# Kernel optimization log

Measured on AMD Instinct MI355X. Metric: run time of the kernel, lower is better.

## Reference

```python
import jax, jax.numpy as jnp
import numpy as np

B, P, E, S = 4, 2048, 4096, 16


def setup_inputs() -> dict:
    key = jax.random.key(0)
    ks = jax.random.split(key, 6)
    return {
        "x": jax.random.normal(ks[0], (B, P, E), dtype=jnp.float32),
        "product": jax.random.normal(ks[1], (P, S), dtype=jnp.float32) * 0.1,
        "person": jax.random.normal(ks[2], (E, S), dtype=jnp.float32) * 0.1,
        "W1": jax.random.normal(ks[3], (2 * S, S), dtype=jnp.float32) * (1.0 / np.sqrt(2 * S)),
        "W2": jax.random.normal(ks[4], (S, S), dtype=jnp.float32) * (1.0 / np.sqrt(S)),
        "W3": jax.random.normal(ks[5], (S, 1), dtype=jnp.float32) * (1.0 / np.sqrt(S)),
    }


def reference(x, product, person, W1, W2, W3):
    # cartesian product concat([pr, pe]) @ W1 == pr @ W1[:S] + pe @ W1[S:]
    # (no bias), so we avoid materializing the (P*E, 2S) concat tensor.
    Wa, Wb = W1[:S], W1[S:]           # each (S, S)
    h1 = jnp.tanh(
        (product @ Wa)[:, None, :] +  # (P, 1, S)
        (person @ Wb)[None, :, :]     # (1, E, S)
    )                                  # (P, E, S)
    h2 = jnp.tanh(h1 @ W2)            # (P, E, S)
    z = (h2 @ W3)[..., 0]             # (P, E)
    score = jnp.where(z >= 0, z, 0.1 * z)  # leaky relu, alpha=0.1
    return score[None, :, :] * x      # (B, P, E)
```

## Files before the change

kernel.cpp:

```cpp
#include <hip/hip_runtime.h>

#define BB 4
#define PP 2048
#define EE 4096
#define SS 16
#define TP 16
#define EBLK 256

typedef __fp16 v2h __attribute__((ext_vector_type(2)));
typedef __fp16 v4h __attribute__((ext_vector_type(4)));
typedef float  v4f __attribute__((ext_vector_type(4)));

static __device__ __forceinline__ float tanh_poly(float x) {
    float t = x * x;
    float u = fmaf(0.010163f, t, -0.046163f);
    u = fmaf(u, t, 0.130718f);
    u = fmaf(u, t, -0.332932f);
    u = fmaf(u, t, 0.999980f);
    return x * u;
}

__global__ __launch_bounds__(256) void precompute_ab(
    const float* __restrict__ product, const float* __restrict__ person,
    const float* __restrict__ W1, float* __restrict__ a, float* __restrict__ b)
{
    int row = blockIdx.x * blockDim.x + threadIdx.x;
    if (row >= PP + EE) return;
    const bool  is_p  = row < PP;
    const float* in   = is_p ? (product + (size_t)row * SS)
                             : (person  + (size_t)(row - PP) * SS);
    const float* W    = is_p ? W1 : (W1 + SS * SS);
    float*       orow = is_p ? (a + (size_t)row * SS)
                             : (b + (size_t)(row - PP) * SS);
    float v[SS];
#pragma unroll
    for (int k = 0; k < SS; ++k) v[k] = in[k];
#pragma unroll
    for (int j = 0; j < SS; ++j) {
        float acc = 0.0f;
#pragma unroll
        for (int k = 0; k < SS; ++k) acc = fmaf(v[k], W[k * SS + j], acc);
        orow[j] = acc;
    }
}

__global__ __launch_bounds__(256) void score_mul(
    const float* __restrict__ x, const float* __restrict__ a,
    const float* __restrict__ b, const float* __restrict__ W2,
    const float* __restrict__ W3, float* __restrict__ out)
{
    const int tid  = threadIdx.x;
    const int lane = tid & 63;
    const int n    = lane & 15;
    const int q    = lane >> 4;
    const int q0   = q & 1;
    const int q1   = q >> 1;

    const int eown  = blockIdx.x * EBLK + tid;
    const int ebase = blockIdx.x * EBLK + (tid & ~63);
    const int p0 = blockIdx.y * TP;

    const size_t PLANE = (size_t)PP * EE;

    float4 brg[4];
#pragma unroll
    for (int g = 0; g < 4; ++g)
        brg[g] = *(const float4*)(b + (size_t)(ebase + g*16 + n) * SS + q*4);

    v4h w2a;
    {
        v2h lo = __builtin_amdgcn_cvt_pkrtz(W2[(q*4+0)*SS + n], W2[(q*4+1)*SS + n]);
        v2h hi = __builtin_amdgcn_cvt_pkrtz(W2[(q*4+2)*SS + n], W2[(q*4+3)*SS + n]);
        w2a[0]=lo[0]; w2a[1]=lo[1]; w2a[2]=hi[0]; w2a[3]=hi[1];
    }

    float4 w3v = ((const float4*)W3)[q];
    const float w3r[4] = {w3v.x, w3v.y, w3v.z, w3v.w};

    size_t base0 = (size_t)p0 * EE + (size_t)eown;
    const float* __restrict__ xp0 = x   + base0;
    float*       __restrict__ op0 = out + base0;

    const v4f z4 = {0.f, 0.f, 0.f, 0.f};

    float xv[BB];
#pragma unroll
    for (int bb2 = 0; bb2 < BB; ++bb2)
        xv[bb2] = xp0[(size_t)bb2 * PLANE];
    float4 av = *(const float4*)(a + (size_t)p0 * SS + q*4);

    for (int ip = 0; ip < TP; ++ip) {
        const size_t off = (size_t)ip * EE;

        float  xn[BB];
        float4 an;
        if (ip + 1 < TP) {
            const size_t offn = off + EE;
#pragma unroll
            for (int bb2 = 0; bb2 < BB; ++bb2)
                xn[bb2] = xp0[(size_t)bb2 * PLANE + offn];
            an = *(const float4*)(a + (size_t)(p0 + ip + 1) * SS + q*4);
        } else {
            an = av;
#pragma unroll
            for (int bb2 = 0; bb2 < BB; ++bb2) xn[bb2] = xv[bb2];
        }

        v4h bfrag[4];
#pragma unroll
        for (int g = 0; g < 4; ++g) {
            float t0 = tanh_poly(av.x + brg[g].x);
            float t1 = tanh_poly(av.y + brg[g].y);
            float t2 = tanh_poly(av.z + brg[g].z);
            float t3 = tanh_poly(av.w + brg[g].w);
            v2h lo = __builtin_amdgcn_cvt_pkrtz(t0, t1);
            v2h hi = __builtin_amdgcn_cvt_pkrtz(t2, t3);
            bfrag[g][0]=lo[0]; bfrag[g][1]=lo[1]; bfrag[g][2]=hi[0]; bfrag[g][3]=hi[1];
        }

        float P[4];
#pragma unroll
        for (int g = 0; g < 4; ++g) {
            v4f acc = __builtin_amdgcn_mfma_f32_16x16x16f16(w2a, bfrag[g], z4, 0, 0, 0);
            float s = 0.f;
#pragma unroll
            for (int r = 0; r < 4; ++r)
                s = fmaf(tanh_poly(acc[r]), w3r[r], s);
            P[g] = s;
        }

        float S1[2];
#pragma unroll
        for (int g1 = 0; g1 < 2; ++g1) {
            float send = q0 ? P[2*g1 + 0] : P[2*g1 + 1];
            float keep = q0 ? P[2*g1 + 1] : P[2*g1 + 0];
            S1[g1] = keep + __shfl_xor(send, 16);
        }
        {
            float send = q1 ? S1[0] : S1[1];
            float keep = q1 ? S1[1] : S1[0];
            float z = keep + __shfl_xor(send, 32);

            float sc = fmaxf(z, 0.f) + 0.1f * fminf(z, 0.f);

#pragma unroll
            for (int bb2 = 0; bb2 < BB; ++bb2)
                __builtin_nontemporal_store(sc * xv[bb2],
                                            op0 + (size_t)bb2 * PLANE + off);
        }

        av = an;
#pragma unroll
        for (int bb2 = 0; bb2 < BB; ++bb2) xv[bb2] = xn[bb2];
    }
}

extern "C" void kernel_launch(void* const* d_in, const int* in_sizes, int n_in,
                              void* d_out, int out_size, void* d_ws, size_t ws_size,
                              hipStream_t stream)
{
    const float* x       = (const float*)d_in[0];
    const float* product = (const float*)d_in[1];
    const float* person  = (const float*)d_in[2];
    const float* W1      = (const float*)d_in[3];
    const float* W2      = (const float*)d_in[4];
    const float* W3      = (const float*)d_in[5];
    float* out = (float*)d_out;

    float* a = (float*)d_ws;
    float* b = a + (size_t)PP * SS;

    dim3 g1((PP + EE + 255) / 256);
    precompute_ab<<<g1, 256, 0, stream>>>(product, person, W1, a, b);

    dim3 g2(EE / EBLK, PP / TP);
    score_mul<<<g2, 256, 0, stream>>>(x, a, b, W2, W3, out);
}
```

Baseline: 270.1 us.

## Process two product rows per iteration, drop software prefetch and nontemporal stores

The main loop now handles two p rows per iteration, loading both rows' x values up front and interleaving the tanh, MFMA and shuffle chains for the two rows to expose more independent work. The explicit one-ahead register prefetch of x and a is removed, and output writes change from nontemporal stores to ordinary stores. This trades the explicit pipelining for more instruction-level parallelism within each iteration, at the cost of higher register pressure. The ordinary stores may also pollute the cache on a streaming output.

```diff
diff --git a/kernel.cpp b/kernel.cpp
--- a/kernel.cpp
+++ b/kernel.cpp
@@ -71,7 +71,7 @@
     {
         v2h lo = __builtin_amdgcn_cvt_pkrtz(W2[(q*4+0)*SS + n], W2[(q*4+1)*SS + n]);
         v2h hi = __builtin_amdgcn_cvt_pkrtz(W2[(q*4+2)*SS + n], W2[(q*4+3)*SS + n]);
-        w2a[0]=lo[0]; w2a[1]=lo[1]; w2a[2]=hi[0]; w2a[3]=hi[1];
+        w2a = __builtin_shufflevector(lo, hi, 0, 1, 2, 3);
     }
 
     float4 w3v = ((const float4*)W3)[q];
@@ -83,75 +83,80 @@
 
     const v4f z4 = {0.f, 0.f, 0.f, 0.f};
 
-    float xv[BB];
+    for (int ip = 0; ip < TP; ip += 2) {
+        const size_t offA = (size_t)ip * EE;
+        const size_t offB = offA + EE;
+
+        float xA[BB], xB[BB];
 #pragma unroll
-    for (int bb2 = 0; bb2 < BB; ++bb2)
-        xv[bb2] = xp0[(size_t)bb2 * PLANE];
-    float4 av = *(const float4*)(a + (size_t)p0 * SS + q*4);
-
-    for (int ip = 0; ip < TP; ++ip) {
-        const size_t off = (size_t)ip * EE;
-
-        float  xn[BB];
-        float4 an;
-        if (ip + 1 < TP) {
-            const size_t offn = off + EE;
-#pragma unroll
-            for (int bb2 = 0; bb2 < BB; ++bb2)
-                xn[bb2] = xp0[(size_t)bb2 * PLANE + offn];
-            an = *(const float4*)(a + (size_t)(p0 + ip + 1) * SS + q*4);
-        } else {
-            an = av;
-#pragma unroll
-            for (int bb2 = 0; bb2 < BB; ++bb2) xn[bb2] = xv[bb2];
+        for (int bb2 = 0; bb2 < BB; ++bb2) {
+            xA[bb2] = xp0[(size_t)bb2 * PLANE + offA];
+            xB[bb2] = xp0[(size_t)bb2 * PLANE + offB];
         }
 
-        v4h bfrag[4];
+        float4 avA = *(const float4*)(a + (size_t)(p0 + ip)     * SS + q*4);
+        float4 avB = *(const float4*)(a + (size_t)(p0 + ip + 1) * SS + q*4);
+
+        v4h bfA[4], bfB[4];
 #pragma unroll
         for (int g = 0; g < 4; ++g) {
-            float t0 = tanh_poly(av.x + brg[g].x);
-            float t1 = tanh_poly(av.y + brg[g].y);
-            float t2 = tanh_poly(av.z + brg[g].z);
-            float t3 = tanh_poly(av.w + brg[g].w);
-            v2h lo = __builtin_amdgcn_cvt_pkrtz(t0, t1);
-            v2h hi = __builtin_amdgcn_cvt_pkrtz(t2, t3);
-            bfrag[g][0]=lo[0]; bfrag[g][1]=lo[1]; bfrag[g][2]=hi[0]; bfrag[g][3]=hi[1];
+            float a0 = tanh_poly(avA.x + brg[g].x);
+            float a1 = tanh_poly(avA.y + brg[g].y);
+            float a2 = tanh_poly(avA.z + brg[g].z);
+            float a3 = tanh_poly(avA.w + brg[g].w);
+            v2h alo = __builtin_amdgcn_cvt_pkrtz(a0, a1);
+            v2h ahi = __builtin_amdgcn_cvt_pkrtz(a2, a3);
+            bfA[g] = __builtin_shufflevector(alo, ahi, 0, 1, 2, 3);
+
+            float b0 = tanh_poly(avB.x + brg[g].x);
+            float b1 = tanh_poly(avB.y + brg[g].y);
+            float b2 = tanh_poly(avB.z + brg[g].z);
+            float b3 = tanh_poly(avB.w + brg[g].w);
+            v2h blo = __builtin_amdgcn_cvt_pkrtz(b0, b1);
+            v2h bhi = __builtin_amdgcn_cvt_pkrtz(b2, b3);
+            bfB[g] = __builtin_shufflevector(blo, bhi, 0, 1, 2, 3);
         }
 
-        float P[4];
+        float PA[4], PB[4];
 #pragma unroll
         for (int g = 0; g < 4; ++g) {
-            v4f acc = __builtin_amdgcn_mfma_f32_16x16x16f16(w2a, bfrag[g], z4, 0, 0, 0);
-            float s = 0.f;
+            v4f accA = __builtin_amdgcn_mfma_f32_16x16x16f16(w2a, bfA[g], z4, 0, 0, 0);
+            v4f accB = __builtin_amdgcn_mfma_f32_16x16x16f16(w2a, bfB[g], z4, 0, 0, 0);
+            float sA = 0.f, sB = 0.f;
 #pragma unroll
-            for (int r = 0; r < 4; ++r)
-                s = fmaf(tanh_poly(acc[r]), w3r[r], s);
-            P[g] = s;
+            for (int r = 0; r < 4; ++r) {
+                sA = fmaf(tanh_poly(accA[r]), w3r[r], sA);
+                sB = fmaf(tanh_poly(accB[r]), w3r[r], sB);
+            }
+            PA[g] = sA;
+            PB[g] = sB;
         }
 
-        float S1[2];
+        float S1A[2], S1B[2];
 #pragma unroll
         for (int g1 = 0; g1 < 2; ++g1) {
-            float send = q0 ? P[2*g1 + 0] : P[2*g1 + 1];
-            float keep = q0 ? P[2*g1 + 1] : P[2*g1 + 0];
-            S1[g1] = keep + __shfl_xor(send, 16);
+            float sendA = q0 ? PA[2*g1 + 0] : PA[2*g1 + 1];
+            float keepA = q0 ? PA[2*g1 + 1] : PA[2*g1 + 0];
+            S1A[g1] = keepA + __shfl_xor(sendA, 16);
+            float sendB = q0 ? PB[2*g1 + 0] : PB[2*g1 + 1];
+            float keepB = q0 ? PB[2*g1 + 1] : PB[2*g1 + 0];
+            S1B[g1] = keepB + __shfl_xor(sendB, 16);
         }
-        {
-            float send = q1 ? S1[0] : S1[1];
-            float keep = q1 ? S1[1] : S1[0];
-            float z = keep + __shfl_xor(send, 32);
+        float sendA = q1 ? S1A[0] : S1A[1];
+        float keepA = q1 ? S1A[1] : S1A[0];
+        float zA    = keepA + __shfl_xor(sendA, 32);
+        float sendB = q1 ? S1B[0] : S1B[1];
+        float keepB = q1 ? S1B[1] : S1B[0];
+        float zB    = keepB + __shfl_xor(sendB, 32);
 
-            float sc = fmaxf(z, 0.f) + 0.1f * fminf(z, 0.f);
+        float scA = fmaxf(zA, 0.f) + 0.1f * fminf(zA, 0.f);
+        float scB = fmaxf(zB, 0.f) + 0.1f * fminf(zB, 0.f);
 
 #pragma unroll
-            for (int bb2 = 0; bb2 < BB; ++bb2)
-                __builtin_nontemporal_store(sc * xv[bb2],
-                                            op0 + (size_t)bb2 * PLANE + off);
+        for (int bb2 = 0; bb2 < BB; ++bb2) {
+            op0[(size_t)bb2 * PLANE + offA] = scA * xA[bb2];
+            op0[(size_t)bb2 * PLANE + offB] = scB * xB[bb2];
         }
-
-        av = an;
-#pragma unroll
-        for (int bb2 = 0; bb2 < BB; ++bb2) xv[bb2] = xn[bb2];
     }
 }
 
```

Result: faster. 262.0 us (-3.0%).

## Widen per-thread work to four elements with float4 loads and stores

Applied to the files above, without the earlier changes.

Each wave now covers 256 E columns (16 MFMA groups) instead of 64, and each thread handles 4 consecutive E elements. x loads and out stores become float4 vectorized, with a lane-shuffle redistribution of scores. The b fragments are stored as fp16 to save registers, TP drops to 8, and an occupancy hint is added. The software prefetch of x is removed and nontemporal stores are replaced by plain stores. The change trades more shuffles and lower b precision for wider memory transactions.

```diff
diff --git a/kernel.cpp b/kernel.cpp
--- a/kernel.cpp
+++ b/kernel.cpp
@@ -4,8 +4,8 @@
 #define PP 2048
 #define EE 4096
 #define SS 16
-#define TP 16
-#define EBLK 256
+#define TP 8
+#define EPB 1024
 
 typedef __fp16 v2h __attribute__((ext_vector_type(2)));
 typedef __fp16 v4h __attribute__((ext_vector_type(4)));
@@ -44,114 +44,115 @@
     }
 }
 
-__global__ __launch_bounds__(256) void score_mul(
+__global__ __launch_bounds__(256, 4) void score_mul(
     const float* __restrict__ x, const float* __restrict__ a,
     const float* __restrict__ b, const float* __restrict__ W2,
     const float* __restrict__ W3, float* __restrict__ out)
 {
     const int tid  = threadIdx.x;
     const int lane = tid & 63;
+    const int wid  = tid >> 6;
     const int n    = lane & 15;
     const int q    = lane >> 4;
     const int q0   = q & 1;
     const int q1   = q >> 1;
 
-    const int eown  = blockIdx.x * EBLK + tid;
-    const int ebase = blockIdx.x * EBLK + (tid & ~63);
-    const int p0 = blockIdx.y * TP;
-
+    const int ebase = blockIdx.x * EPB + wid * 256;
+    const int e0    = ebase + lane * 4;
+    const int p0    = blockIdx.y * TP;
     const size_t PLANE = (size_t)PP * EE;
 
-    float4 brg[4];
+    v4h brg[16];
 #pragma unroll
-    for (int g = 0; g < 4; ++g)
-        brg[g] = *(const float4*)(b + (size_t)(ebase + g*16 + n) * SS + q*4);
+    for (int g = 0; g < 16; ++g) {
+        float4 bv = *(const float4*)(b + (size_t)(ebase + g*16 + n) * SS + q*4);
+        v2h lo = __builtin_amdgcn_cvt_pkrtz(bv.x, bv.y);
+        v2h hi = __builtin_amdgcn_cvt_pkrtz(bv.z, bv.w);
+        brg[g] = __builtin_shufflevector(lo, hi, 0, 1, 2, 3);
+    }
 
     v4h w2a;
     {
         v2h lo = __builtin_amdgcn_cvt_pkrtz(W2[(q*4+0)*SS + n], W2[(q*4+1)*SS + n]);
         v2h hi = __builtin_amdgcn_cvt_pkrtz(W2[(q*4+2)*SS + n], W2[(q*4+3)*SS + n]);
-        w2a[0]=lo[0]; w2a[1]=lo[1]; w2a[2]=hi[0]; w2a[3]=hi[1];
+        w2a = __builtin_shufflevector(lo, hi, 0, 1, 2, 3);
     }
 
-    float4 w3v = ((const float4*)W3)[q];
-    const float w3r[4] = {w3v.x, w3v.y, w3v.z, w3v.w};
+    const float4 w3v = ((const float4*)W3)[q];
 
-    size_t base0 = (size_t)p0 * EE + (size_t)eown;
-    const float* __restrict__ xp0 = x   + base0;
-    float*       __restrict__ op0 = out + base0;
+    const float* __restrict__ xp0 = x   + (size_t)p0 * EE + e0;
+    float*       __restrict__ op0 = out + (size_t)p0 * EE + e0;
 
-    const v4f z4 = {0.f, 0.f, 0.f, 0.f};
-
-    float xv[BB];
-#pragma unroll
-    for (int bb2 = 0; bb2 < BB; ++bb2)
-        xv[bb2] = xp0[(size_t)bb2 * PLANE];
-    float4 av = *(const float4*)(a + (size_t)p0 * SS + q*4);
+    const v4f zero4 = {0.f, 0.f, 0.f, 0.f};
+    const int srcb = ((lane >> 2) & 3) * 16 + (lane & 3) * 4;
 
     for (int ip = 0; ip < TP; ++ip) {
         const size_t off = (size_t)ip * EE;
 
-        float  xn[BB];
-        float4 an;
-        if (ip + 1 < TP) {
-            const size_t offn = off + EE;
+        float4 av = *(const float4*)(a + (size_t)(p0 + ip) * SS + q*4);
+
+        float4 xv[BB];
 #pragma unroll
-            for (int bb2 = 0; bb2 < BB; ++bb2)
-                xn[bb2] = xp0[(size_t)bb2 * PLANE + offn];
-            an = *(const float4*)(a + (size_t)(p0 + ip + 1) * SS + q*4);
-        } else {
-            an = av;
+        for (int bb2 = 0; bb2 < BB; ++bb2)
+            xv[bb2] = *(const float4*)(xp0 + (size_t)bb2 * PLANE + off);
+
+        float P[16];
 #pragma unroll
-            for (int bb2 = 0; bb2 < BB; ++bb2) xn[bb2] = xv[bb2];
-        }
-
-        v4h bfrag[4];
-#pragma unroll
-        for (int g = 0; g < 4; ++g) {
-            float t0 = tanh_poly(av.x + brg[g].x);
-            float t1 = tanh_poly(av.y + brg[g].y);
-            float t2 = tanh_poly(av.z + brg[g].z);
-            float t3 = tanh_poly(av.w + brg[g].w);
+        for (int g = 0; g < 16; ++g) {
+            float t0 = tanh_poly(av.x + (float)brg[g][0]);
+            float t1 = tanh_poly(av.y + (float)brg[g][1]);
+            float t2 = tanh_poly(av.z + (float)brg[g][2]);
+            float t3 = tanh_poly(av.w + (float)brg[g][3]);
             v2h lo = __builtin_amdgcn_cvt_pkrtz(t0, t1);
             v2h hi = __builtin_amdgcn_cvt_pkrtz(t2, t3);
-            bfrag[g][0]=lo[0]; bfrag[g][1]=lo[1]; bfrag[g][2]=hi[0]; bfrag[g][3]=hi[1];
-        }
-
-        float P[4];
-#pragma unroll
-        for (int g = 0; g < 4; ++g) {
-            v4f acc = __builtin_amdgcn_mfma_f32_16x16x16f16(w2a, bfrag[g], z4, 0, 0, 0);
+            v4h bf = __builtin_shufflevector(lo, hi, 0, 1, 2, 3);
+            v4f acc = __builtin_amdgcn_mfma_f32_16x16x16f16(w2a, bf, zero4, 0, 0, 0);
             float s = 0.f;
-#pragma unroll
-            for (int r = 0; r < 4; ++r)
-                s = fmaf(tanh_poly(acc[r]), w3r[r], s);
+            s = fmaf(tanh_poly(acc[0]), w3v.x, s);
+            s = fmaf(tanh_poly(acc[1]), w3v.y, s);
+            s = fmaf(tanh_poly(acc[2]), w3v.z, s);
+            s = fmaf(tanh_poly(acc[3]), w3v.w, s);
             P[g] = s;
         }
 
-        float S1[2];
+        float S1[8];
 #pragma unroll
-        for (int g1 = 0; g1 < 2; ++g1) {
-            float send = q0 ? P[2*g1 + 0] : P[2*g1 + 1];
-            float keep = q0 ? P[2*g1 + 1] : P[2*g1 + 0];
-            S1[g1] = keep + __shfl_xor(send, 16);
+        for (int m = 0; m < 8; ++m) {
+            float send = q0 ? P[2*m]   : P[2*m+1];
+            float keep = q0 ? P[2*m+1] : P[2*m];
+            S1[m] = keep + __shfl_xor(send, 16);
         }
-        {
-            float send = q1 ? S1[0] : S1[1];
-            float keep = q1 ? S1[1] : S1[0];
-            float z = keep + __shfl_xor(send, 32);
+        float F[4];
+#pragma unroll
+        for (int c = 0; c < 4; ++c) {
+            float send = q1 ? S1[2*c]   : S1[2*c+1];
+            float keep = q1 ? S1[2*c+1] : S1[2*c];
+            F[c] = keep + __shfl_xor(send, 32);
+        }
 
-            float sc = fmaxf(z, 0.f) + 0.1f * fminf(z, 0.f);
+        float sc[4];
+#pragma unroll
+        for (int j = 0; j < 4; ++j) {
+            const int srcl = srcb + j;
+            float t0 = __shfl(F[0], srcl);
+            float t1 = __shfl(F[1], srcl);
+            float t2 = __shfl(F[2], srcl);
+            float t3 = __shfl(F[3], srcl);
+            float lo = q0 ? t1 : t0;
+            float hi = q0 ? t3 : t2;
+            float z  = q1 ? hi : lo;
+            sc[j] = fmaxf(z, 0.f) + 0.1f * fminf(z, 0.f);
+        }
 
 #pragma unroll
-            for (int bb2 = 0; bb2 < BB; ++bb2)
-                __builtin_nontemporal_store(sc * xv[bb2],
-                                            op0 + (size_t)bb2 * PLANE + off);
+        for (int bb2 = 0; bb2 < BB; ++bb2) {
+            float4 ov;
+            ov.x = sc[0] * xv[bb2].x;
+            ov.y = sc[1] * xv[bb2].y;
+            ov.z = sc[2] * xv[bb2].z;
+            ov.w = sc[3] * xv[bb2].w;
+            *(float4*)(op0 + (size_t)bb2 * PLANE + off) = ov;
         }
-
-        av = an;
-#pragma unroll
-        for (int bb2 = 0; bb2 < BB; ++bb2) xv[bb2] = xn[bb2];
     }
 }
 
@@ -173,6 +174,6 @@
     dim3 g1((PP + EE + 255) / 256);
     precompute_ab<<<g1, 256, 0, stream>>>(product, person, W1, a, b);
 
-    dim3 g2(EE / EBLK, PP / TP);
+    dim3 g2(EE / EPB, PP / TP);
     score_mul<<<g2, 256, 0, stream>>>(x, a, b, W2, W3, out);
 }
```

Result: faster. 259.7 us (-3.8%).
